# Kernel optimization log

Hardware: AMD Instinct MI355X
Metric: run time of the kernel (lower is better)

Reference implementation:

```python
import jax, jax.numpy as jnp
import numpy as np

K, N_PER, D_IN, D_OUT = 16, 16384, 256, 256
N = K * N_PER


def setup_inputs() -> dict:
    key = jax.random.key(0)
    k1, k2, k3 = jax.random.split(key, 3)
    x = jax.random.normal(k1, (K, N_PER, D_IN), dtype=jnp.float32)
    w = jax.random.normal(k2, (K, D_OUT, D_IN), dtype=jnp.float32) * (1.0 / np.sqrt(D_IN))
    # collect order: permutation mapping grouped-by-type rows -> global neuron order
    perm = jax.random.permutation(k3, N).astype(jnp.int32)
    return {"x": x, "w": w, "perm": perm}


def reference(x, w, perm):
    # per-type unique linear: y[k,n,o] = sum_d x[k,n,d] * w[k,o,d]
    y = jnp.einsum('knd,kod->kno', x, w)          # [K, N_PER, D_OUT]
    y = y.reshape(N, D_OUT)[perm]                 # collect into unified neuron order
    return jnp.tanh(y)
```

## Files before the change

### kernel.cpp

```cpp
#include <hip/hip_runtime.h>
#include <hip/hip_bf16.h>

#define KT    16
#define NPER  16384
#define DIN   256
#define DOUT  256
#define NTOT  (KT * NPER)

typedef __attribute__((ext_vector_type(8))) short  short8;
typedef __attribute__((ext_vector_type(4))) float  f32x4;
typedef __attribute__((ext_vector_type(4))) unsigned int uint32x4;

__device__ __forceinline__ unsigned short f2bf(float f) {
    unsigned int u = __float_as_uint(f);
    u += 0x7fffu + ((u >> 16) & 1u);
    return (unsigned short)(u >> 16);
}

__device__ __forceinline__ float fast_tanh(float y) {
    float a = fabsf(y);
    float t = __expf(-2.0f * a);
    float r = (1.0f - t) * __builtin_amdgcn_rcpf(1.0f + t);
    return copysignf(r, y);
}


__global__ void prep_w(const float* __restrict__ w, unsigned short* __restrict__ wbf) {
    int i = blockIdx.x * blockDim.x + threadIdx.x;
    float4 v = ((const float4*)w)[i];
    unsigned int p0 = (unsigned int)f2bf(v.x) | ((unsigned int)f2bf(v.y) << 16);
    unsigned int p1 = (unsigned int)f2bf(v.z) | ((unsigned int)f2bf(v.w) << 16);
    ((uint2*)wbf)[i] = make_uint2(p0, p1);
}

__global__ void prep_inv(const int* __restrict__ perm, int* __restrict__ inv) {
    int i = blockIdx.x * blockDim.x + threadIdx.x;
    inv[perm[i]] = i;
}


__launch_bounds__(512, 4)
__global__ void gemm_scatter(const float* __restrict__ x,
                             const unsigned short* __restrict__ wbf,
                             const int* __restrict__ inv,
                             float* __restrict__ out) {
    __shared__ unsigned short aLds[128 * 72];
    __shared__ unsigned short bLds[256 * 72];
    __shared__ int invLds[128];

    const int tid = threadIdx.x;
    const int bid = blockIdx.x;
    const int kt  = bid >> 7;
    const int rt  = bid & 127;

    const float*          xblk = x   + (size_t)(kt * NPER + rt * 128) * DIN;
    const unsigned short* wblk = wbf + (size_t)kt * DOUT * DIN;

    if (tid < 128) invLds[tid] = inv[kt * NPER + rt * 128 + tid];

    const int lane = tid & 63;
    const int wv   = tid >> 6;
    const int wm   = wv & 1;
    const int wn   = wv >> 1;
    const int lo   = lane & 15;
    const int hi   = lane >> 4;

    f32x4 acc[4][4];
#pragma unroll
    for (int i = 0; i < 4; i++)
#pragma unroll
        for (int j = 0; j < 4; j++) acc[i][j] = (f32x4){0.f, 0.f, 0.f, 0.f};

    for (int s = 0; s < 4; ++s) {
        const int d0 = s * 64;

#pragma unroll
        for (int r8 = 0; r8 < 2; r8++) {
            int idx = tid + r8 * 512;
            int row = idx >> 3, c8 = idx & 7;
            const float4* p = (const float4*)(xblk + row * DIN + d0 + c8 * 8);
            float4 v0 = p[0];
            float4 v1 = p[1];
            uint32x4 pk;
            pk.x = (unsigned int)f2bf(v0.x) | ((unsigned int)f2bf(v0.y) << 16);
            pk.y = (unsigned int)f2bf(v0.z) | ((unsigned int)f2bf(v0.w) << 16);
            pk.z = (unsigned int)f2bf(v1.x) | ((unsigned int)f2bf(v1.y) << 16);
            pk.w = (unsigned int)f2bf(v1.z) | ((unsigned int)f2bf(v1.w) << 16);
            *(uint32x4*)&aLds[row * 72 + c8 * 8] = pk;
        }
#pragma unroll
        for (int r8 = 0; r8 < 4; r8++) {
            int idx = tid + r8 * 512;
            int row = idx >> 3, c8 = idx & 7;
            uint32x4 v = *(const uint32x4*)(wblk + row * DIN + d0 + c8 * 8);
            *(uint32x4*)&bLds[row * 72 + c8 * 8] = v;
        }
        __syncthreads();

#pragma unroll
        for (int ks = 0; ks < 2; ++ks) {
            const int k0 = ks * 32;
            short8 af[4], bfr[4];
#pragma unroll
            for (int i = 0; i < 4; i++)
                af[i] = *(const short8*)&aLds[(wm * 64 + i * 16 + lo) * 72 + k0 + hi * 8];
#pragma unroll
            for (int j = 0; j < 4; j++)
                bfr[j] = *(const short8*)&bLds[(wn * 64 + j * 16 + lo) * 72 + k0 + hi * 8];
#pragma unroll
            for (int i = 0; i < 4; i++)
#pragma unroll
                for (int j = 0; j < 4; j++)
                    acc[i][j] = __builtin_amdgcn_mfma_f32_16x16x32_bf16(
                        af[i], bfr[j], acc[i][j], 0, 0, 0);
        }
        __syncthreads();
    }

#pragma unroll
    for (int i = 0; i < 4; i++) {
#pragma unroll
        for (int r = 0; r < 4; r++) {
            int rowL = wm * 64 + i * 16 + hi * 4 + r;
            size_t orow = (size_t)invLds[rowL];
            float* op = out + orow * DOUT;
#pragma unroll
            for (int j = 0; j < 4; j++) {
                int col = wn * 64 + j * 16 + lo;
                op[col] = fast_tanh(acc[i][j][r]);
            }
        }
    }
}


extern "C" void kernel_launch(void* const* d_in, const int* in_sizes, int n_in,
                              void* d_out, int out_size, void* d_ws, size_t ws_size,
                              hipStream_t stream) {
    const float* x    = (const float*)d_in[0];
    const float* w    = (const float*)d_in[1];
    const int*   perm = (const int*)d_in[2];
    float*       out  = (float*)d_out;

    unsigned short* wbf = (unsigned short*)d_ws;
    int*            inv = (int*)((char*)d_ws + (size_t)2 * 1024 * 1024);

    prep_w  <<<1024, 256, 0, stream>>>(w, wbf);
    prep_inv<<<1024, 256, 0, stream>>>(perm, inv);
    gemm_scatter<<<KT * 128, 512, 0, stream>>>(x, wbf, inv, out);
}
```

Measured before the change: 457.1 us.

## Load MFMA fragments directly from global memory, dropping LDS staging and barriers

The GEMM no longer stages x and the bf16 weights through shared memory. Each lane now loads its own MFMA A and B fragments straight from global memory, converts x to bf16 in registers, and the loop over K is fully unrolled with no __syncthreads. The permutation indices are also read with vector loads from global memory instead of through LDS. This removes the LDS traffic and the barriers, but each x element is now loaded by four waves instead of once per block, so the kernel leans on L1/L2 for reuse and issues more global loads.

Result: slower. 609.7 us (+33.4%).

```diff
diff --git a/kernel.cpp b/kernel.cpp
--- a/kernel.cpp
+++ b/kernel.cpp
@@ -11,10 +11,23 @@
 typedef __attribute__((ext_vector_type(4))) float  f32x4;
 typedef __attribute__((ext_vector_type(4))) unsigned int uint32x4;
 
+__device__ __forceinline__ unsigned int bfbits(unsigned int u) {
+    return (u + 0x7fffu + ((u >> 16) & 1u)) >> 16;
+}
+
+__device__ __forceinline__ short8 pack8(uint32x4 a, uint32x4 b) {
+    uint32x4 r;
+    r.x = bfbits(a.x) | (bfbits(a.y) << 16);
+    r.y = bfbits(a.z) | (bfbits(a.w) << 16);
+    r.z = bfbits(b.x) | (bfbits(b.y) << 16);
+    r.w = bfbits(b.z) | (bfbits(b.w) << 16);
+    short8 s;
+    __builtin_memcpy(&s, &r, sizeof(s));
+    return s;
+}
+
 __device__ __forceinline__ unsigned short f2bf(float f) {
-    unsigned int u = __float_as_uint(f);
-    u += 0x7fffu + ((u >> 16) & 1u);
-    return (unsigned short)(u >> 16);
+    return (unsigned short)bfbits(__float_as_uint(f));
 }
 
 __device__ __forceinline__ float fast_tanh(float y) {
@@ -44,19 +57,10 @@
                              const unsigned short* __restrict__ wbf,
                              const int* __restrict__ inv,
                              float* __restrict__ out) {
-    __shared__ unsigned short aLds[128 * 72];
-    __shared__ unsigned short bLds[256 * 72];
-    __shared__ int invLds[128];
-
-    const int tid = threadIdx.x;
-    const int bid = blockIdx.x;
-    const int kt  = bid >> 7;
-    const int rt  = bid & 127;
-
-    const float*          xblk = x   + (size_t)(kt * NPER + rt * 128) * DIN;
-    const unsigned short* wblk = wbf + (size_t)kt * DOUT * DIN;
-
-    if (tid < 128) invLds[tid] = inv[kt * NPER + rt * 128 + tid];
+    const int tid  = threadIdx.x;
+    const int bid  = blockIdx.x;
+    const int kt   = bid >> 7;
+    const int rt   = bid & 127;
 
     const int lane = tid & 63;
     const int wv   = tid >> 6;
@@ -65,70 +69,53 @@
     const int lo   = lane & 15;
     const int hi   = lane >> 4;
 
+    const int rowbase = rt * 128;
+
+    const float* xb = x
+        + ((size_t)(kt * NPER + rowbase + wm * 64 + lo)) * DIN + hi * 8;
+    const unsigned short* wb = wbf
+        + (size_t)kt * DOUT * DIN + (size_t)(wn * 64 + lo) * DIN + hi * 8;
+
     f32x4 acc[4][4];
 #pragma unroll
     for (int i = 0; i < 4; i++)
 #pragma unroll
         for (int j = 0; j < 4; j++) acc[i][j] = (f32x4){0.f, 0.f, 0.f, 0.f};
 
-    for (int s = 0; s < 4; ++s) {
-        const int d0 = s * 64;
+#pragma unroll
+    for (int kk = 0; kk < 8; ++kk) {
+        const int k0 = kk * 32;
+
+        short8 af[4], bf[4];
+#pragma unroll
+        for (int i = 0; i < 4; ++i) {
+            const uint32x4* p = (const uint32x4*)(xb + (size_t)(i * 16) * DIN + k0);
+            uint32x4 v0 = p[0];
+            uint32x4 v1 = p[1];
+            af[i] = pack8(v0, v1);
+        }
+#pragma unroll
+        for (int j = 0; j < 4; ++j)
+            bf[j] = *(const short8*)(wb + (size_t)(j * 16) * DIN + k0);
 
 #pragma unroll
-        for (int r8 = 0; r8 < 2; r8++) {
-            int idx = tid + r8 * 512;
-            int row = idx >> 3, c8 = idx & 7;
-            const float4* p = (const float4*)(xblk + row * DIN + d0 + c8 * 8);
-            float4 v0 = p[0];
-            float4 v1 = p[1];
-            uint32x4 pk;
-            pk.x = (unsigned int)f2bf(v0.x) | ((unsigned int)f2bf(v0.y) << 16);
-            pk.y = (unsigned int)f2bf(v0.z) | ((unsigned int)f2bf(v0.w) << 16);
-            pk.z = (unsigned int)f2bf(v1.x) | ((unsigned int)f2bf(v1.y) << 16);
-            pk.w = (unsigned int)f2bf(v1.z) | ((unsigned int)f2bf(v1.w) << 16);
-            *(uint32x4*)&aLds[row * 72 + c8 * 8] = pk;
-        }
+        for (int i = 0; i < 4; ++i)
 #pragma unroll
-        for (int r8 = 0; r8 < 4; r8++) {
-            int idx = tid + r8 * 512;
-            int row = idx >> 3, c8 = idx & 7;
-            uint32x4 v = *(const uint32x4*)(wblk + row * DIN + d0 + c8 * 8);
-            *(uint32x4*)&bLds[row * 72 + c8 * 8] = v;
-        }
-        __syncthreads();
-
-#pragma unroll
-        for (int ks = 0; ks < 2; ++ks) {
-            const int k0 = ks * 32;
-            short8 af[4], bfr[4];
-#pragma unroll
-            for (int i = 0; i < 4; i++)
-                af[i] = *(const short8*)&aLds[(wm * 64 + i * 16 + lo) * 72 + k0 + hi * 8];
-#pragma unroll
-            for (int j = 0; j < 4; j++)
-                bfr[j] = *(const short8*)&bLds[(wn * 64 + j * 16 + lo) * 72 + k0 + hi * 8];
-#pragma unroll
-            for (int i = 0; i < 4; i++)
-#pragma unroll
-                for (int j = 0; j < 4; j++)
-                    acc[i][j] = __builtin_amdgcn_mfma_f32_16x16x32_bf16(
-                        af[i], bfr[j], acc[i][j], 0, 0, 0);
-        }
-        __syncthreads();
+            for (int j = 0; j < 4; ++j)
+                acc[i][j] = __builtin_amdgcn_mfma_f32_16x16x32_bf16(
+                    af[i], bf[j], acc[i][j], 0, 0, 0);
     }
 
 #pragma unroll
-    for (int i = 0; i < 4; i++) {
+    for (int i = 0; i < 4; ++i) {
+        const int4 iv = *(const int4*)&inv[kt * NPER + rowbase + wm * 64 + i * 16 + hi * 4];
+        const int orow[4] = {iv.x, iv.y, iv.z, iv.w};
 #pragma unroll
-        for (int r = 0; r < 4; r++) {
-            int rowL = wm * 64 + i * 16 + hi * 4 + r;
-            size_t orow = (size_t)invLds[rowL];
-            float* op = out + orow * DOUT;
+        for (int r = 0; r < 4; ++r) {
+            float* op = out + (size_t)orow[r] * DOUT + wn * 64 + lo;
 #pragma unroll
-            for (int j = 0; j < 4; j++) {
-                int col = wn * 64 + j * 16 + lo;
-                op[col] = fast_tanh(acc[i][j][r]);
-            }
+            for (int j = 0; j < 4; ++j)
+                op[j * 16] = fast_tanh(acc[i][j][r]);
         }
     }
 }
```

## Double-buffer GEMM K-loop with direct global-to-LDS loads for weights

Applied to the files above, without the earlier changes.

The K loop now uses 8 stages of 32 columns with double-buffered LDS tiles. The next stage's x rows are prefetched into registers and converted to bf16 after the current MFMAs run. The weight tile is copied straight into LDS with global_load_lds, using a byte-chunk mapping that matches the padded 40-element row stride. This hides global load latency behind MFMA work and drops one barrier per stage, at the cost of more, smaller stages and some wasted loads into the padding.

After: 525.4 us. 14.9% more time.

```diff
diff --git a/kernel.cpp b/kernel.cpp
--- a/kernel.cpp
+++ b/kernel.cpp
@@ -1,20 +1,23 @@
 #include <hip/hip_runtime.h>
-#include <hip/hip_bf16.h>
 
 #define KT    16
 #define NPER  16384
 #define DIN   256
 #define DOUT  256
-#define NTOT  (KT * NPER)
+
+#define BK      32
+#define NSTAGE  8
+#define LSTRIDE 40
 
 typedef __attribute__((ext_vector_type(8))) short  short8;
 typedef __attribute__((ext_vector_type(4))) float  f32x4;
 typedef __attribute__((ext_vector_type(4))) unsigned int uint32x4;
 
+__device__ __forceinline__ unsigned int bfbits(unsigned int u) {
+    return (u + 0x7fffu + ((u >> 16) & 1u)) >> 16;
+}
 __device__ __forceinline__ unsigned short f2bf(float f) {
-    unsigned int u = __float_as_uint(f);
-    u += 0x7fffu + ((u >> 16) & 1u);
-    return (unsigned short)(u >> 16);
+    return (unsigned short)bfbits(__float_as_uint(f));
 }
 
 __device__ __forceinline__ float fast_tanh(float y) {
@@ -23,6 +26,11 @@
     float r = (1.0f - t) * __builtin_amdgcn_rcpf(1.0f + t);
     return copysignf(r, y);
 }
+
+#define GLDS16(gsrc, ldst)                                                        \
+    __builtin_amdgcn_global_load_lds(                                             \
+        (const __attribute__((address_space(1))) void*)(gsrc),                    \
+        (__attribute__((address_space(3))) void*)(ldst), 16, 0, 0)
 
 
 __global__ void prep_w(const float* __restrict__ w, unsigned short* __restrict__ wbf) {
@@ -44,8 +52,8 @@
                              const unsigned short* __restrict__ wbf,
                              const int* __restrict__ inv,
                              float* __restrict__ out) {
-    __shared__ unsigned short aLds[128 * 72];
-    __shared__ unsigned short bLds[256 * 72];
+    __shared__ unsigned short aLds[2][128 * LSTRIDE];
+    __shared__ unsigned short bLds[2][256 * LSTRIDE];
     __shared__ int invLds[128];
 
     const int tid = threadIdx.x;
@@ -65,54 +73,75 @@
     const int lo   = lane & 15;
     const int hi   = lane >> 4;
 
+    const int arow = tid >> 2;
+    const int ac8  = tid & 3;
+    const float* aSrc = xblk + (size_t)arow * DIN + ac8 * 8;
+    const int    aOff = arow * LSTRIDE + ac8 * 8;
+
+    const int c0 = wv * 2, c1 = c0 + 1, c2 = 16 + wv;
+    const int b0 = c0 * 1024 + lane * 16;
+    const int b1 = c1 * 1024 + lane * 16;
+    const int b2 = c2 * 1024 + lane * 16;
+    const unsigned short* bSrc0 = wblk + (size_t)(b0 / 80) * DIN + (b0 % 80) / 2;
+    const unsigned short* bSrc1 = wblk + (size_t)(b1 / 80) * DIN + (b1 % 80) / 2;
+    const unsigned short* bSrc2 = wblk + (size_t)(b2 / 80) * DIN + (b2 % 80) / 2;
+    const int bo0 = c0 * 512, bo1 = c1 * 512, bo2 = c2 * 512;
+
     f32x4 acc[4][4];
 #pragma unroll
     for (int i = 0; i < 4; i++)
 #pragma unroll
         for (int j = 0; j < 4; j++) acc[i][j] = (f32x4){0.f, 0.f, 0.f, 0.f};
 
-    for (int s = 0; s < 4; ++s) {
-        const int d0 = s * 64;
+    {
+        float4 a0 = ((const float4*)aSrc)[0];
+        float4 a1 = ((const float4*)aSrc)[1];
+        GLDS16(bSrc0, &bLds[0][bo0]);
+        GLDS16(bSrc1, &bLds[0][bo1]);
+        if (wv < 4) GLDS16(bSrc2, &bLds[0][bo2]);
+        uint32x4 pk;
+        pk.x = bfbits(__float_as_uint(a0.x)) | (bfbits(__float_as_uint(a0.y)) << 16);
+        pk.y = bfbits(__float_as_uint(a0.z)) | (bfbits(__float_as_uint(a0.w)) << 16);
+        pk.z = bfbits(__float_as_uint(a1.x)) | (bfbits(__float_as_uint(a1.y)) << 16);
+        pk.w = bfbits(__float_as_uint(a1.z)) | (bfbits(__float_as_uint(a1.w)) << 16);
+        *(uint32x4*)&aLds[0][aOff] = pk;
+    }
+    __syncthreads();
 
+    for (int s = 0; s < NSTAGE; ++s) {
+        const int cur = s & 1;
+
+        float4 a0, a1;
+        if (s < NSTAGE - 1) {
+            const int d0n = (s + 1) * BK;
+            a0 = ((const float4*)(aSrc + d0n))[0];
+            a1 = ((const float4*)(aSrc + d0n))[1];
+            GLDS16(bSrc0 + d0n, &bLds[cur ^ 1][bo0]);
+            GLDS16(bSrc1 + d0n, &bLds[cur ^ 1][bo1]);
+            if (wv < 4) GLDS16(bSrc2 + d0n, &bLds[cur ^ 1][bo2]);
+        }
+
+        short8 af[4], bfr[4];
 #pragma unroll
-        for (int r8 = 0; r8 < 2; r8++) {
-            int idx = tid + r8 * 512;
-            int row = idx >> 3, c8 = idx & 7;
-            const float4* p = (const float4*)(xblk + row * DIN + d0 + c8 * 8);
-            float4 v0 = p[0];
-            float4 v1 = p[1];
-            uint32x4 pk;
-            pk.x = (unsigned int)f2bf(v0.x) | ((unsigned int)f2bf(v0.y) << 16);
-            pk.y = (unsigned int)f2bf(v0.z) | ((unsigned int)f2bf(v0.w) << 16);
-            pk.z = (unsigned int)f2bf(v1.x) | ((unsigned int)f2bf(v1.y) << 16);
-            pk.w = (unsigned int)f2bf(v1.z) | ((unsigned int)f2bf(v1.w) << 16);
-            *(uint32x4*)&aLds[row * 72 + c8 * 8] = pk;
-        }
+        for (int i = 0; i < 4; i++)
+            af[i] = *(const short8*)&aLds[cur][(wm * 64 + i * 16 + lo) * LSTRIDE + hi * 8];
 #pragma unroll
-        for (int r8 = 0; r8 < 4; r8++) {
-            int idx = tid + r8 * 512;
-            int row = idx >> 3, c8 = idx & 7;
-            uint32x4 v = *(const uint32x4*)(wblk + row * DIN + d0 + c8 * 8);
-            *(uint32x4*)&bLds[row * 72 + c8 * 8] = v;
-        }
-        __syncthreads();
-
+        for (int j = 0; j < 4; j++)
+            bfr[j] = *(const short8*)&bLds[cur][(wn * 64 + j * 16 + lo) * LSTRIDE + hi * 8];
 #pragma unroll
-        for (int ks = 0; ks < 2; ++ks) {
-            const int k0 = ks * 32;
-            short8 af[4], bfr[4];
-#pragma unroll
-            for (int i = 0; i < 4; i++)
-                af[i] = *(const short8*)&aLds[(wm * 64 + i * 16 + lo) * 72 + k0 + hi * 8];
+        for (int i = 0; i < 4; i++)
 #pragma unroll
             for (int j = 0; j < 4; j++)
-                bfr[j] = *(const short8*)&bLds[(wn * 64 + j * 16 + lo) * 72 + k0 + hi * 8];
-#pragma unroll
-            for (int i = 0; i < 4; i++)
-#pragma unroll
-                for (int j = 0; j < 4; j++)
-                    acc[i][j] = __builtin_amdgcn_mfma_f32_16x16x32_bf16(
-                        af[i], bfr[j], acc[i][j], 0, 0, 0);
+                acc[i][j] = __builtin_amdgcn_mfma_f32_16x16x32_bf16(
+                    af[i], bfr[j], acc[i][j], 0, 0, 0);
+
+        if (s < NSTAGE - 1) {
+            uint32x4 pk;
+            pk.x = bfbits(__float_as_uint(a0.x)) | (bfbits(__float_as_uint(a0.y)) << 16);
+            pk.y = bfbits(__float_as_uint(a0.z)) | (bfbits(__float_as_uint(a0.w)) << 16);
+            pk.z = bfbits(__float_as_uint(a1.x)) | (bfbits(__float_as_uint(a1.y)) << 16);
+            pk.w = bfbits(__float_as_uint(a1.z)) | (bfbits(__float_as_uint(a1.w)) << 16);
+            *(uint32x4*)&aLds[cur ^ 1][aOff] = pk;
         }
         __syncthreads();
     }
```
